# Performance work log

Hardware: AMD Instinct MI355X
Metric: run time of the kernel (lower is better)

Reference implementation:

```python
import jax, jax.numpy as jnp
import numpy as np


def _conv(x, w, b=None, stride=1, pad=0, groups=1):
    out = jax.lax.conv_general_dilated(
        x, w, (stride, stride), [(pad, pad), (pad, pad)],
        feature_group_count=groups,
        dimension_numbers=('NCHW', 'OIHW', 'NCHW'))
    return out if b is None else out + b[None, :, None, None]


def _lrelu(z):
    return jnp.where(z >= 0, z, 0.1 * z)


def _bn(z, g, b, m, v):
    # eval-mode batchnorm, eps=1e-5
    scale = (g / jnp.sqrt(v + 1e-5))[None, :, None, None]
    return (z - m[None, :, None, None]) * scale + b[None, :, None, None]


def setup_inputs() -> dict:
    key = jax.random.key(0)
    ks = jax.random.split(key, 32)
    s = 0.05
    r = lambda k, sh: jax.random.normal(k, sh, jnp.float32) * s
    inp = {}
    inp['x'] = jax.random.normal(ks[0], (4, 64, 256, 256), jnp.float32)
    inp['y'] = jax.random.normal(ks[1], (4, 64, 64, 64), jnp.float32)
    # Encoder convs + BN (eval stats)
    inp['ew1'] = r(ks[2], (128, 64, 3, 3)); inp['eb1'] = r(ks[3], (128,))
    inp['ebn1_g'] = jnp.ones((128,), jnp.float32); inp['ebn1_b'] = jnp.zeros((128,), jnp.float32)
    inp['ebn1_m'] = jnp.zeros((128,), jnp.float32); inp['ebn1_v'] = jnp.ones((128,), jnp.float32)
    inp['ew2'] = r(ks[4], (256, 128, 3, 3)); inp['eb2'] = r(ks[5], (256,))
    inp['ebn2_g'] = jnp.ones((256,), jnp.float32); inp['ebn2_b'] = jnp.zeros((256,), jnp.float32)
    inp['ebn2_m'] = jnp.zeros((256,), jnp.float32); inp['ebn2_v'] = jnp.ones((256,), jnp.float32)
    # Encoder MLP (torch Linear: [out, in])
    inp['mw1'] = r(ks[6], (256, 256)); inp['mb1'] = r(ks[7], (256,))
    inp['mw2'] = r(ks[8], (256, 256)); inp['mb2'] = r(ks[9], (256,))
    # kernel-prediction head (no bias)
    inp['kw1'] = r(ks[10], (128, 256))
    inp['kw2'] = r(ks[11], (64 * 3 * 3, 128))
    # 1x1 conv after dynamic conv
    inp['cw'] = r(ks[12], (64, 64, 1, 1)); inp['cb'] = r(ks[13], (64,))
    # CA layer (reduction=8 -> 256//8 = 32 mid channels, no bias)
    inp['caw1'] = r(ks[14], (32, 64, 1, 1)); inp['caw2'] = r(ks[15], (64, 32, 1, 1))
    # conv1 (3x3) and conv2 (3x3 stride 2)
    inp['c1w'] = r(ks[16], (64, 64, 3, 3)); inp['c1b'] = r(ks[17], (64,))
    inp['c2w'] = r(ks[18], (64, 64, 3, 3)); inp['c2b'] = r(ks[19], (64,))
    # shared ResBlock (two 3x3 convs + residual)
    inp['r1w'] = r(ks[20], (64, 64, 3, 3)); inp['r1b'] = r(ks[21], (64,))
    inp['r2w'] = r(ks[22], (64, 64, 3, 3)); inp['r2b'] = r(ks[23], (64,))
    return inp


def reference(x, y, ew1, eb1, ebn1_g, ebn1_b, ebn1_m, ebn1_v,
              ew2, eb2, ebn2_g, ebn2_b, ebn2_m, ebn2_v,
              mw1, mb1, mw2, mb2, kw1, kw2, cw, cb, caw1, caw2,
              c1w, c1b, c2w, c2b, r1w, r1b, r2w, r2b):
    b, c, h, w = x.shape
    k = 3

    # ---- Encoder(y) -> degradation embedding [b, 256] ----
    f = _lrelu(_bn(_conv(y, ew1, eb1, stride=2, pad=1), ebn1_g, ebn1_b, ebn1_m, ebn1_v))
    f = _lrelu(_bn(_conv(f, ew2, eb2, stride=1, pad=0), ebn2_g, ebn2_b, ebn2_m, ebn2_v))
    f = jnp.mean(f, axis=(2, 3))                       # AdaptiveAvgPool2d(1)
    emb = _lrelu(f @ mw1.T + mb1) @ mw2.T + mb2        # [b, 256]

    # ---- dynamic per-sample depthwise kernel [b*c, 1, k, k] ----
    kern = _lrelu(emb @ kw1.T) @ kw2.T                 # [b, 64*k*k]
    kern = kern.reshape(b * c, 1, k, k)

    # ---- dynamic depthwise conv (groups = b*c) ----
    dyn = _lrelu(_conv(x.reshape(1, b * c, h, w), kern, pad=(k - 1) // 2, groups=b * c))
    dyn = _conv(dyn.reshape(b, c, h, w), cw, cb)       # 1x1 conv

    # ---- channel attention branch ----
    att = jax.nn.relu(_conv(_lrelu(_conv(x, caw1)), caw2))
    da = dyn + x * att

    # ---- DAB body ----
    out = _lrelu(da)
    out = _conv(out, c1w, c1b, pad=1) + x              # [b,64,256,256]

    def resb(z):
        return z + _conv(jax.nn.relu(_conv(z, r1w, r1b, pad=1)), r2w, r2b, pad=1)

    out2 = resb(_conv(out, c2w, c2b, stride=2, pad=1))   # [b,64,128,128]
    out3 = resb(_conv(out2, c2w, c2b, stride=2, pad=1))  # [b,64,64,64]
    return (out, out2, out3)
```

## Files before the change

### kernel.cpp

```cpp
#include <hip/hip_runtime.h>
#include <hip/hip_bf16.h>
#include <cstddef>
#include <cstdint>

#define DEV __device__ __forceinline__

DEV float lrelu_f(float z){ return z >= 0.f ? z : 0.1f*z; }

typedef __bf16 bf16x8 __attribute__((ext_vector_type(8)));
typedef float  f32x4  __attribute__((ext_vector_type(4)));
typedef unsigned short u16x8 __attribute__((ext_vector_type(8)));

DEV unsigned short bf_bits(float v){
    __hip_bfloat16 h = __float2bfloat16(v);
    unsigned short s; __builtin_memcpy(&s, &h, 2); return s;
}
DEV unsigned short bf_bits(__hip_bfloat16 v){
    unsigned short s; __builtin_memcpy(&s, &v, 2); return s;
}
DEV float u16_to_f(unsigned short s){
    unsigned int u = ((unsigned int)s) << 16;
    float f; __builtin_memcpy(&f, &u, 4); return f;
}
DEV int xswz(int bx, int n){ return (bx & 7) * (n >> 3) + (bx >> 3); }

__global__ __launch_bounds__(256) void k_prep_all(
    const float* __restrict__ c1w,
    const float* __restrict__ ew1, const float* __restrict__ bn1g, const float* __restrict__ bn1v,
    const float* __restrict__ ew2, const float* __restrict__ bn2g, const float* __restrict__ bn2v,
    const float* __restrict__ cw, const float* __restrict__ caw1, const float* __restrict__ caw2,
    __hip_bfloat16* __restrict__ wpA, __hip_bfloat16* __restrict__ wp1,
    __hip_bfloat16* __restrict__ wp2, __hip_bfloat16* __restrict__ wpF)
{
    const int blk = blockIdx.x, tid = threadIdx.x;
    if (blk < 144){
        int i = blk*256 + tid;
        int e = i & 7, coA = (i>>3)&63, g = (i>>9)&3, f = i>>11;
        int ch = (f>=9)?1:0, pos = f-9*ch;
        wpA[i] = __float2bfloat16(c1w[coA*576 + (ch*32+g*8+e)*9 + pos]);
    } else if (blk < 432){
        int i = (blk-144)*256 + tid;
        int e = i & 7, co = (i>>3)&127, g = (i>>10)&3, f = i>>12;
        int ch = (f>=9)?1:0, pos = f-9*ch;
        float s = bn1g[co] / sqrtf(bn1v[co] + 1e-5f);
        wp1[i] = __float2bfloat16(ew1[co*576 + (ch*32+g*8+e)*9 + pos] * s);
    } else if (blk < 1584){
        int i = (blk-432)*256 + tid;
        int e = i & 7, co = (i>>3)&255, g = (i>>11)&3, f = i>>13;
        int ch = f/9, pos = f-9*ch;
        float s = bn2g[co] / sqrtf(bn2v[co] + 1e-5f);
        wp2[i] = __float2bfloat16(ew2[co*1152 + (ch*32+g*8+e)*9 + pos] * s);
    } else {
        int i = (blk-1584)*256 + tid;
        if (i < 4096){
            int e = i&7, co = (i>>3)&63, g = (i>>9)&3, ch = i>>11;
            wpF[i] = __float2bfloat16(cw[co*64 + ch*32 + g*8 + e]);
        } else if (i < 6144){
            int j = i - 4096;
            int e = j&7, co = (j>>3)&31, g = (j>>8)&3, ch = j>>10;
            wpF[i] = __float2bfloat16(caw1[co*64 + ch*32 + g*8 + e]);
        } else {
            int j = i - 6144;
            int e = j&7, co = (j>>3)&63, g = j>>9;
            wpF[i] = __float2bfloat16(caw2[co*32 + g*8 + e]);
        }
    }
}

__global__ __launch_bounds__(256) void k_wprepB(
    const float* __restrict__ c2w, const float* __restrict__ r1w,
    const float* __restrict__ r2w, __hip_bfloat16* __restrict__ wpB)
{
    int i = blockIdx.x*256 + threadIdx.x;
    int sel = i / 36864;
    int j   = i - sel*36864;
    const float* w = (sel==0) ? c2w : (sel==1) ? r1w : r2w;
    int e = j & 7, coA = (j>>3)&63, g = (j>>9)&3, f = j>>11;
    int ch = (f>=9)?1:0, pos = f-9*ch;
    wpB[i] = __float2bfloat16(w[coA*576 + (ch*32+g*8+e)*9 + pos]);
}

__global__ __launch_bounds__(256) void k_enc1m(
    const float* __restrict__ y, const __hip_bfloat16* __restrict__ wp1,
    const float* __restrict__ eb1, const float* __restrict__ bng,
    const float* __restrict__ bnb, const float* __restrict__ bnm,
    const float* __restrict__ bnv, __hip_bfloat16* __restrict__ e1b)
{
    __shared__ __align__(16) char lA[9*33*128];
    const int tid = threadIdx.x;
    const int wid = tid >> 6, lane = tid & 63;
    const int l15 = lane & 15, lg = lane >> 4;
    const int b = blockIdx.y, tile = blockIdx.x;
    const int toh = (tile >> 1) * 4;
    const int tow = (tile & 1) * 16;
    const int row0 = toh*2 - 1, col0 = tow*2 - 1;

    for (int i = tid; i < 9*33*64; i += 256){
        int c  = i % 33;
        int t  = i / 33;
        int r  = t % 9;
        int ci = t / 9;
        int ih = row0 + r, iw = col0 + c;
        unsigned short bits = 0;
        if (ih >= 0 && ih < 64 && iw >= 0 && iw < 64)
            bits = bf_bits(y[((size_t)(b*64+ci) << 12) + ih*64 + iw]);
        *(unsigned short*)(lA + ((r*33+c)*8 + ((ci>>3) ^ (c&7)))*16 + (ci&7)*2) = bits;
    }
    __syncthreads();

    f32x4 acc[2][4];
    #pragma unroll
    for (int s = 0; s < 2; ++s)
        #pragma unroll
        for (int n = 0; n < 4; ++n) acc[s][n] = (f32x4){0.f,0.f,0.f,0.f};

    #pragma unroll
    for (int ch = 0; ch < 2; ++ch){
        #pragma unroll
        for (int pos = 0; pos < 9; ++pos){
            const int f = ch*9 + pos;
            const int kh = pos/3, kw = pos - 3*(pos/3);
            bf16x8 bx[4];
            #pragma unroll
            for (int n = 0; n < 4; ++n){
                const int rr = n*2 + kh, cc = l15*2 + kw;
                bx[n] = *(const bf16x8*)(lA + ((rr*33+cc)*8 + ((ch*4+lg) ^ (cc&7)))*16);
            }
            #pragma unroll
            for (int s = 0; s < 2; ++s){
                const int coA = wid*32 + s*16 + l15;
                bf16x8 aw = *(const bf16x8*)(wp1 + ((size_t)(f*4 + lg)*128 + coA)*8);
                #pragma unroll
                for (int n = 0; n < 4; ++n)
                    acc[s][n] = __builtin_amdgcn_mfma_f32_16x16x32_bf16(aw, bx[n], acc[s][n], 0,0,0);
            }
        }
    }

    #pragma unroll
    for (int s = 0; s < 2; ++s){
        #pragma unroll
        for (int r = 0; r < 4; ++r){
            const int co = wid*32 + s*16 + lg*4 + r;
            float sb = bng[co] / sqrtf(bnv[co] + 1e-5f);
            float bs = (eb1[co] - bnm[co])*sb + bnb[co];
            #pragma unroll
            for (int n = 0; n < 4; ++n){
                int oh = toh + n, ow = tow + l15;
                e1b[((size_t)(b*128+co) << 10) + oh*32 + ow]
                    = __float2bfloat16(lrelu_f(acc[s][n][r] + bs));
            }
        }
    }
}

__global__ __launch_bounds__(256) void k_enc2m(
    const __hip_bfloat16* __restrict__ e1b, const __hip_bfloat16* __restrict__ wp2,
    const float* __restrict__ bias, const float* __restrict__ g_,
    const float* __restrict__ bb, const float* __restrict__ m_,
    const float* __restrict__ v_, float* __restrict__ partial)
{
    __shared__ __align__(16) char lA[6*18*16*16];
    const int tid = threadIdx.x;
    const int wid = tid >> 6, lane = tid & 63;
    const int l15 = lane & 15, lg = lane >> 4;
    const int b = blockIdx.y, tile = blockIdx.x;
    const int toh = (tile >> 1) * 4;
    const int tow = (tile & 1) * 16;

    for (int i = tid; i < 13824; i += 256){
        int c  = i % 18;
        int t  = i / 18;
        int r  = t % 6;
        int ci = t / 6;
        int ih = toh + r, iw = tow + c;
        unsigned short bits = 0;
        if (ih < 32 && iw < 32)
            bits = bf_bits(e1b[((size_t)(b*128+ci) << 10) + ih*32 + iw]);
        *(unsigned short*)(lA + ((r*18+c)*16 + ((ci>>3) ^ (c&7)))*16 + (ci&7)*2) = bits;
    }
    __syncthreads();

    f32x4 acc[4][4];
    #pragma unroll
    for (int s = 0; s < 4; ++s)
        #pragma unroll
        for (int n = 0; n < 4; ++n) acc[s][n] = (f32x4){0.f,0.f,0.f,0.f};

    #pragma unroll
    for (int ch = 0; ch < 4; ++ch){
        #pragma unroll
        for (int pos = 0; pos < 9; ++pos){
            const int f = ch*9 + pos;
            const int kh = pos/3, kw = pos - 3*(pos/3);
            bf16x8 bx[4];
            #pragma unroll
            for (int n = 0; n < 4; ++n){
                const int rr = n + kh, cc = l15 + kw;
                bx[n] = *(const bf16x8*)(lA + ((rr*18+cc)*16 + ((ch*4+lg) ^ (cc&7)))*16);
            }
            #pragma unroll
            for (int s = 0; s < 4; ++s){
                const int coA = wid*64 + s*16 + l15;
                bf16x8 aw = *(const bf16x8*)(wp2 + ((size_t)(f*4 + lg)*256 + coA)*8);
                #pragma unroll
                for (int n = 0; n < 4; ++n)
                    acc[s][n] = __builtin_amdgcn_mfma_f32_16x16x32_bf16(aw, bx[n], acc[s][n], 0,0,0);
            }
        }
    }

    const int ow = tow + l15;
    const bool owok = ow < 30;
    #pragma unroll
    for (int s = 0; s < 4; ++s){
        #pragma unroll
        for (int r = 0; r < 4; ++r){
            const int co = wid*64 + s*16 + lg*4 + r;
            float sb = g_[co] / sqrtf(v_[co] + 1e-5f);
            float bs = (bias[co] - m_[co])*sb + bb[co];
            float th = 0.f;
            #pragma unroll
            for (int n = 0; n < 4; ++n){
                if (owok && (toh + n) < 30)
                    th += lrelu_f(acc[s][n][r] + bs);
            }
            th += __shfl_xor(th, 1);
            th += __shfl_xor(th, 2);
            th += __shfl_xor(th, 4);
            th += __shfl_xor(th, 8);
            if (l15 == 0)
                partial[((size_t)(b*16 + tile))*256 + co] = th;
        }
    }
}

__global__ __launch_bounds__(256) void k_mlp(
    const float* __restrict__ partial,
    const float* __restrict__ mw1, const float* __restrict__ mb1,
    const float* __restrict__ mw2, const float* __restrict__ mb2,
    const float* __restrict__ kw1, const float* __restrict__ kw2,
    float* __restrict__ kern)
{
    __shared__ float fs[256], h1[256], emb[256], k1[128];
    int b = blockIdx.x, t = threadIdx.x;
    {
        float s = 0.f;
        #pragma unroll
        for (int tt = 0; tt < 16; ++tt)
            s += partial[((size_t)(b*16 + tt))*256 + t];
        fs[t] = s * (1.f/900.f);
    }
    __syncthreads();
    {
        float acc = mb1[t];
        const float* wr = mw1 + t*256;
        for (int i=0;i<256;++i) acc += fs[i]*wr[i];
        h1[t] = lrelu_f(acc);
    }
    __syncthreads();
    {
        float acc = mb2[t];
        const float* wr = mw2 + t*256;
        for (int i=0;i<256;++i) acc += h1[i]*wr[i];
        emb[t] = acc;
    }
    __syncthreads();
    if (t < 128){
        float acc = 0.f;
        const float* wr = kw1 + t*256;
        for (int i=0;i<256;++i) acc += emb[i]*wr[i];
        k1[t] = lrelu_f(acc);
    }
    __syncthreads();
    for (int o=t; o<576; o+=256){
        float acc = 0.f;
        const float* wr = kw2 + o*128;
        for (int i=0;i<128;++i) acc += k1[i]*wr[i];
        kern[b*576+o] = acc;
    }
}

__global__ __launch_bounds__(256) void k_fuse(
    const float* __restrict__ x, const float* __restrict__ kern,
    const __hip_bfloat16* __restrict__ wpF, const float* __restrict__ cb,
    __hip_bfloat16* __restrict__ buf)
{
    __shared__ __align__(16) char lA [6*18*128];
    __shared__ __align__(16) char lD [64*128];
    __shared__ __align__(16) char lA1[64*64];
    __shared__ float kern_s[576];

    const int tid = threadIdx.x;
    const int wid = tid >> 6, lane = tid & 63;
    const int l15 = lane & 15, lg = lane >> 4;
    const int b = blockIdx.y;
    const int bx = xswz(blockIdx.x, gridDim.x);
    const int toh = (bx >> 4) * 4;
    const int tow = (bx & 15) * 16;
    const int row0 = toh - 1;
    const int col0 = tow - 1;

    const bool cfast = (tow >= 1) && (tow + 20 <= 256);
    for (int i = tid; i < 6*64; i += 256){
        const int ci = i & 63, r = i >> 6;
        const int ih = row0 + r;
        if (ih < 0 || ih >= 256){
            #pragma unroll
            for (int c = 0; c < 18; ++c)
                *(unsigned short*)(lA + ((r*18+c)*8 + ((ci>>3)^(c&7)))*16 + (ci&7)*2) = 0;
        } else {
            const float* srow = x + ((size_t)(b*64+ci) << 16) + ih*256;
            if (cfast){
                float edge = srow[tow-1];
                f32x4 chk[5];
                #pragma unroll
                for (int k = 0; k < 5; ++k)
                    chk[k] = *(const f32x4*)(srow + tow + k*4);
                *(unsigned short*)(lA + ((r*18+0)*8 + ((ci>>3)^0))*16 + (ci&7)*2) = bf_bits(edge);
                #pragma unroll
                for (int c = 1; c < 18; ++c){
                    const int idx = c - 1;
                    unsigned short bits = bf_bits(chk[idx>>2][idx&3]);
                    *(unsigned short*)(lA + ((r*18+c)*8 + ((ci>>3)^(c&7)))*16 + (ci&7)*2) = bits;
                }
            } else {
                #pragma unroll
                for (int c = 0; c < 18; ++c){
                    int iw = col0 + c;
                    unsigned short bits = 0;
                    if (iw >= 0 && iw < 256) bits = bf_bits(srow[iw]);
                    *(unsigned short*)(lA + ((r*18+c)*8 + ((ci>>3)^(c&7)))*16 + (ci&7)*2) = bits;
                }
            }
        }
    }
    for (int i = tid; i < 576; i += 256) kern_s[i] = kern[b*576 + i];
    __syncthreads();

    const int m1 = wid & 1;
    const int nb = (wid >> 1) * 2;
    f32x4 a1acc[2] = {{0.f,0.f,0.f,0.f},{0.f,0.f,0.f,0.f}};
    const int coA1 = m1*16 + l15;
    #pragma unroll
    for (int ch = 0; ch < 2; ++ch){
        bf16x8 aA = *(const bf16x8*)(wpF + 4096 + ((ch*4+lg)*32 + coA1)*8);
        #pragma unroll
        for (int t = 0; t < 2; ++t){
            int n = nb + t;
            int cc = l15 + 1, rr = n + 1;
            bf16x8 bX = *(const bf16x8*)(lA + ((rr*18+cc)*8 + ((ch*4+lg) ^ (cc&7)))*16);
            a1acc[t] = __builtin_amdgcn_mfma_f32_16x16x32_bf16(aA, bX, a1acc[t], 0,0,0);
        }
    }

    {
        const int px = tid & 63;
        const int s0 = tid >> 6;
        const int prow = px >> 4, pcol = px & 15;
        #pragma unroll
        for (int t = 0; t < 2; ++t){
            const int sl = s0 + t*4;
            u16x8 xv[3][3];
            #pragma unroll
            for (int kh = 0; kh < 3; ++kh)
                #pragma unroll
                for (int kw = 0; kw < 3; ++kw){
                    const int r = prow + kh, c = pcol + kw;
                    xv[kh][kw] = *(const u16x8*)(lA + ((r*18+c)*8 + (sl ^ (c&7)))*16);
                }
            u16x8 outv;
            #pragma unroll
            for (int e = 0; e < 8; ++e){
                const int ci = sl*8 + e;
                const float* kr = kern_s + ci*9;
                float acc = 0.f;
                #pragma unroll
                for (int kh = 0; kh < 3; ++kh)
                    #pragma unroll
                    for (int kw = 0; kw < 3; ++kw)
                        acc += u16_to_f(xv[kh][kw][e]) * kr[kh*3+kw];
                outv[e] = bf_bits(lrelu_f(acc));
            }
            *(u16x8*)(lD + (px*8 + (sl ^ (px&7)))*16) = outv;
        }
    }

    #pragma unroll
    for (int t = 0; t < 2; ++t){
        int n = nb + t;
        int px = n*16 + l15;
        #pragma unroll
        for (int r = 0; r < 4; ++r){
            int j = m1*16 + lg*4 + r;
            *(unsigned short*)(lA1 + (px*4 + ((j>>3) ^ (px&3)))*16 + (j&7)*2)
                = bf_bits(lrelu_f(a1acc[t][r]));
        }
    }
    __syncthreads();

    f32x4 dynacc[4] = {{0.f,0.f,0.f,0.f},{0.f,0.f,0.f,0.f},{0.f,0.f,0.f,0.f},{0.f,0.f,0.f,0.f}};
    f32x4 attacc[4] = {{0.f,0.f,0.f,0.f},{0.f,0.f,0.f,0.f},{0.f,0.f,0.f,0.f},{0.f,0.f,0.f,0.f}};
    const int coA = wid*16 + l15;
    #pragma unroll
    for (int ch = 0; ch < 2; ++ch){
        bf16x8 aW = *(const bf16x8*)(wpF + ((ch*4+lg)*64 + coA)*8);
        #pragma unroll
        for (int n = 0; n < 4; ++n){
            int px = n*16 + l15;
            bf16x8 bD = *(const bf16x8*)(lD + (px*8 + ((ch*4+lg) ^ (px&7)))*16);
            dynacc[n] = __builtin_amdgcn_mfma_f32_16x16x32_bf16(aW, bD, dynacc[n], 0,0,0);
        }
    }
    {
        bf16x8 aW2 = *(const bf16x8*)(wpF + 6144 + (lg*64 + coA)*8);
        #pragma unroll
        for (int n = 0; n < 4; ++n){
            int px = n*16 + l15;
            bf16x8 bA1 = *(const bf16x8*)(lA1 + (px*4 + (lg ^ (px&3)))*16);
            attacc[n] = __builtin_amdgcn_mfma_f32_16x16x32_bf16(aW2, bA1, attacc[n], 0,0,0);
        }
    }

    #pragma unroll
    for (int n = 0; n < 4; ++n){
        int oh = toh + n, ow = tow + l15;
        const int rr = n + 1, cc = l15 + 1;
        #pragma unroll
        for (int r = 0; r < 4; ++r){
            int co = wid*16 + lg*4 + r;
            size_t oi = ((size_t)(b*64+co) << 16) + oh*256 + ow;
            float xv = u16_to_f(*(const unsigned short*)(
                lA + ((rr*18+cc)*8 + ((co>>3) ^ (cc&7)))*16 + (co&7)*2));
            float att = fmaxf(attacc[n][r], 0.f);
            float v = lrelu_f(dynacc[n][r] + cb[co] + xv*att);
            buf[oi] = __float2bfloat16(v);
        }
    }
}

template<typename TIN, int STRIDE, int TH, int RESMODE, int ACT, int OUTBF>
__global__ __launch_bounds__(256) void k_conv_mfma(
    const TIN* __restrict__ in, const __hip_bfloat16* __restrict__ wp,
    const float* __restrict__ bias, const void* __restrict__ res,
    void* __restrict__ outp, int H, int W, int Ho, int Wo)
{
    constexpr int ROWS = (STRIDE==1) ? TH+2 : 2*TH+1;
    constexpr int COLS = (STRIDE==1) ? 18 : 33;
    constexpr int EPC  = (sizeof(TIN)==2) ? 8 : 4;
    constexpr int NCH  = (COLS - 1 + EPC - 1) / EPC;
    __shared__ __align__(16) char lA[ROWS*COLS*128];
    const int tid = threadIdx.x;
    const int wid = tid >> 6, lane = tid & 63;
    const int l15 = lane & 15, g = lane >> 4;
    const int b   = blockIdx.y;
    const int bx  = xswz(blockIdx.x, gridDim.x);
    const int tilesW = Wo >> 4;
    const int toh = (bx / tilesW) * TH;
    const int tow = (bx % tilesW) * 16;
    const int row0 = toh*STRIDE - 1;
    const int col0 = tow*STRIDE - 1;

    bf16x8 aw[18];
    const int coA = wid*16 + l15;
    #pragma unroll
    for (int f = 0; f < 18; ++f)
        aw[f] = *(const bf16x8*)(wp + ((f*4 + g)*64 + coA)*8);

    const int base = tow*STRIDE;
    const bool cfast = (base >= 1) && (base + NCH*EPC <= W);
    for (int i = tid; i < ROWS*64; i += 256){
        const int ci = i & 63, r = i >> 6;
        const int ih = row0 + r;
        if (ih < 0 || ih >= H){
            #pragma unroll
            for (int c = 0; c < COLS; ++c)
                *(unsigned short*)(lA + ((r*COLS+c)*8 + ((ci>>3)^(c&7)))*16 + (ci&7)*2) = 0;
        } else {
            const TIN* srow = in + ((size_t)(b*64+ci))*H*W + (size_t)ih*W;
            if (cfast){
                if constexpr (sizeof(TIN) == 2){
                    unsigned short edge = bf_bits(srow[base-1]);
                    u16x8 chk[NCH];
                    #pragma unroll
                    for (int k = 0; k < NCH; ++k)
                        chk[k] = *(const u16x8*)(srow + base + k*8);
                    *(unsigned short*)(lA + ((r*COLS+0)*8 + (ci>>3))*16 + (ci&7)*2) = edge;
                    #pragma unroll
                    for (int c = 1; c < COLS; ++c){
                        const int idx = c - 1;
                        unsigned short bits = chk[idx>>3][idx&7];
                        *(unsigned short*)(lA + ((r*COLS+c)*8 + ((ci>>3)^(c&7)))*16 + (ci&7)*2) = bits;
                    }
                } else {
                    unsigned short edge = bf_bits(srow[base-1]);
                    f32x4 chk[NCH];
                    #pragma unroll
                    for (int k = 0; k < NCH; ++k)
                        chk[k] = *(const f32x4*)(srow + base + k*4);
                    *(unsigned short*)(lA + ((r*COLS+0)*8 + (ci>>3))*16 + (ci&7)*2) = edge;
                    #pragma unroll
                    for (int c = 1; c < COLS; ++c){
                        const int idx = c - 1;
                        unsigned short bits = bf_bits(chk[idx>>2][idx&3]);
                        *(unsigned short*)(lA + ((r*COLS+c)*8 + ((ci>>3)^(c&7)))*16 + (ci&7)*2) = bits;
                    }
                }
            } else {
                #pragma unroll
                for (int c = 0; c < COLS; ++c){
                    int iw = col0 + c;
                    unsigned short bits = 0;
                    if (iw >= 0 && iw < W) bits = bf_bits(srow[iw]);
                    *(unsigned short*)(lA + ((r*COLS+c)*8 + ((ci>>3)^(c&7)))*16 + (ci&7)*2) = bits;
                }
            }
        }
    }
    __syncthreads();

    float bv[4];
    #pragma unroll
    for (int r = 0; r < 4; ++r) bv[r] = bias[wid*16 + g*4 + r];
    const float*          resF = (const float*)res;
    const __hip_bfloat16* resB = (const __hip_bfloat16*)res;

    if constexpr (STRIDE == 1){
        bf16x8 Bw[3][2][3];
        auto ldrow = [&](int rr, int slot){
            #pragma unroll
            for (int ch = 0; ch < 2; ++ch)
                #pragma unroll
                for (int kw = 0; kw < 3; ++kw){
                    const int cc = l15 + kw;
                    Bw[slot][ch][kw] = *(const bf16x8*)(lA + ((rr*COLS + cc)*8 + ((ch*4+g) ^ (cc&7)))*16);
                }
        };
        ldrow(0, 0);
        ldrow(1, 1);
        #pragma unroll
        for (int n = 0; n < TH; ++n){
            ldrow(n+2, (n+2)%3);
            f32x4 acc = {0.f,0.f,0.f,0.f};
            #pragma unroll
            for (int kh = 0; kh < 3; ++kh)
                #pragma unroll
                for (int ch = 0; ch < 2; ++ch)
                    #pragma unroll
                    for (int kw = 0; kw < 3; ++kw)
                        acc = __builtin_amdgcn_mfma_f32_16x16x32_bf16(
                                aw[ch*9 + kh*3 + kw], Bw[(n+kh)%3][ch][kw], acc, 0, 0, 0);
            const int oh = toh + n, ow = tow + l15;
            #pragma unroll
            for (int r = 0; r < 4; ++r){
                int co = wid*16 + g*4 + r;
                size_t oi = ((size_t)(b*64+co)*Ho + oh)*Wo + ow;
                float v = acc[r] + bv[r];
                if (ACT) v = fmaxf(v, 0.f);
                if (RESMODE == 1) v += resF[oi];
                if (RESMODE == 2) v += __bfloat162float(resB[oi]);
                if (OUTBF) ((__hip_bfloat16*)outp)[oi] = __float2bfloat16(v);
                else       ((float*)outp)[oi] = v;
            }
        }
    } else {
        #pragma unroll
        for (int n = 0; n < TH; ++n){
            f32x4 acc = {0.f,0.f,0.f,0.f};
            #pragma unroll
            for (int ch = 0; ch < 2; ++ch)
                #pragma unroll
                for (int pos = 0; pos < 9; ++pos){
                    const int kh = pos/3, kw = pos - 3*(pos/3);
                    const int cc = l15*STRIDE + kw;
                    const int rr = n*STRIDE + kh;
                    bf16x8 bx2 = *(const bf16x8*)(lA + ((rr*COLS + cc)*8 + ((ch*4+g) ^ (cc&7)))*16);
                    acc = __builtin_amdgcn_mfma_f32_16x16x32_bf16(aw[ch*9+pos], bx2, acc, 0, 0, 0);
                }
            const int oh = toh + n, ow = tow + l15;
            #pragma unroll
            for (int r = 0; r < 4; ++r){
                int co = wid*16 + g*4 + r;
                size_t oi = ((size_t)(b*64+co)*Ho + oh)*Wo + ow;
                float v = acc[r] + bv[r];
                if (ACT) v = fmaxf(v, 0.f);
                if (RESMODE == 1) v += resF[oi];
                if (RESMODE == 2) v += __bfloat162float(resB[oi]);
                if (OUTBF) ((__hip_bfloat16*)outp)[oi] = __float2bfloat16(v);
                else       ((float*)outp)[oi] = v;
            }
        }
    }
}

extern "C" void kernel_launch(void* const* d_in, const int* in_sizes, int n_in,
                              void* d_out, int out_size, void* d_ws, size_t ws_size,
                              hipStream_t stream) {
    const float* x    = (const float*)d_in[0];
    const float* y    = (const float*)d_in[1];
    const float* ew1  = (const float*)d_in[2];
    const float* eb1  = (const float*)d_in[3];
    const float* bn1g = (const float*)d_in[4];
    const float* bn1b = (const float*)d_in[5];
    const float* bn1m = (const float*)d_in[6];
    const float* bn1v = (const float*)d_in[7];
    const float* ew2  = (const float*)d_in[8];
    const float* eb2  = (const float*)d_in[9];
    const float* bn2g = (const float*)d_in[10];
    const float* bn2b = (const float*)d_in[11];
    const float* bn2m = (const float*)d_in[12];
    const float* bn2v = (const float*)d_in[13];
    const float* mw1  = (const float*)d_in[14];
    const float* mb1  = (const float*)d_in[15];
    const float* mw2  = (const float*)d_in[16];
    const float* mb2  = (const float*)d_in[17];
    const float* kw1  = (const float*)d_in[18];
    const float* kw2  = (const float*)d_in[19];
    const float* cw   = (const float*)d_in[20];
    const float* cb   = (const float*)d_in[21];
    const float* caw1 = (const float*)d_in[22];
    const float* caw2 = (const float*)d_in[23];
    const float* c1w  = (const float*)d_in[24];
    const float* c1b  = (const float*)d_in[25];
    const float* c2w  = (const float*)d_in[26];
    const float* c2b  = (const float*)d_in[27];
    const float* r1w  = (const float*)d_in[28];
    const float* r1b  = (const float*)d_in[29];
    const float* r2w  = (const float*)d_in[30];
    const float* r2b  = (const float*)d_in[31];

    char* wsc = (char*)d_ws;
    __hip_bfloat16* buf = (__hip_bfloat16*)wsc;
    __hip_bfloat16* e1b = (__hip_bfloat16*)wsc;
    __hip_bfloat16* wp2 = (__hip_bfloat16*)(wsc + 2097152);
    float*          part= (float*)(wsc + 2686976);
    __hip_bfloat16* t2  = (__hip_bfloat16*)wsc;
    __hip_bfloat16* u2  = (__hip_bfloat16*)(wsc + 8388608);
    __hip_bfloat16* t3  = (__hip_bfloat16*)(wsc + 16777216);
    __hip_bfloat16* u3  = (__hip_bfloat16*)(wsc + 18874368);
    __hip_bfloat16* wpB = (__hip_bfloat16*)(wsc + 29360128);
    __hip_bfloat16* wpB0= wpB;
    __hip_bfloat16* wpB1= wpB + 36864;
    __hip_bfloat16* wpB2= wpB + 73728;
    float*          kern= (float*)(wsc + 33558528);

    float* ob   = (float*)d_out;
    float* ob1  = ob + 16777216;
    float* ob2  = ob + 20971520;
    __hip_bfloat16* wpF = (__hip_bfloat16*)((char*)d_out + 83886080);
    __hip_bfloat16* wp1 = (__hip_bfloat16*)((char*)d_out + 84934656);
    __hip_bfloat16* wpA = (__hip_bfloat16*)((char*)d_out + 87932928);

    k_prep_all<<<dim3(1616),256,0,stream>>>(c1w, ew1, bn1g, bn1v, ew2, bn2g, bn2v,
                                            cw, caw1, caw2, wpA, wp1, wp2, wpF);
    k_enc1m<<<dim3(16,4),256,0,stream>>>(y, wp1, eb1, bn1g, bn1b, bn1m, bn1v, e1b);
    k_enc2m<<<dim3(16,4),256,0,stream>>>(e1b, wp2, eb2, bn2g, bn2b, bn2m, bn2v, part);
    k_mlp<<<dim3(4),256,0,stream>>>(part, mw1, mb1, mw2, mb2, kw1, kw2, kern);
    k_fuse<<<dim3(1024,4),256,0,stream>>>(x, kern, wpF, cb, buf);

    k_conv_mfma<__hip_bfloat16,1,8,1,0,0><<<dim3(512,4),256,0,stream>>>(buf, wpA, c1b, x, ob, 256,256,256,256);
    k_wprepB<<<dim3(432),256,0,stream>>>(c2w, r1w, r2w, wpB);
    k_conv_mfma<float,2,2,0,0,1><<<dim3(512,4),256,0,stream>>>(ob, wpB0, c2b, nullptr, t2, 256,256,128,128);
    k_conv_mfma<__hip_bfloat16,1,8,0,1,1><<<dim3(128,4),256,0,stream>>>(t2, wpB1, r1b, nullptr, u2, 128,128,128,128);
    k_conv_mfma<__hip_bfloat16,1,8,2,0,0><<<dim3(128,4),256,0,stream>>>(u2, wpB2, r2b, t2, ob1, 128,128,128,128);
    k_conv_mfma<float,2,2,0,0,1><<<dim3(128,4),256,0,stream>>>(ob1, wpB0, c2b, nullptr, t3, 128,128,64,64);
    k_conv_mfma<__hip_bfloat16,1,8,0,1,1><<<dim3(32,4),256,0,stream>>>(t3, wpB1, r1b, nullptr, u3, 64,64,64,64);
    k_conv_mfma<__hip_bfloat16,1,8,2,0,0><<<dim3(32,4),256,0,stream>>>(u3, wpB2, r2b, t3, ob2, 64,64,64,64);
}
```

Measured before the change: 350.2 us.

## Compute dynamic depthwise conv via block-diagonal MFMA and pad attention LDS rows

Replaces the scalar per-thread depthwise 3x3 convolution in the fused kernel with MFMA instructions. A sparse A operand holds each output channel's kernel tap at a single K position, so each MFMA performs a diagonal (depthwise) product over 16 channels. The attention LDS buffer row stride is also padded from 4 to 5 16-byte slots, presumably to reduce bank conflicts. The MFMA path wastes most of its multiply work on zeros and adds a scattered LDS write pattern for the result, in exchange for removing the per-thread FMA loops and their register pressure.

```diff
diff --git a/kernel.cpp b/kernel.cpp
--- a/kernel.cpp
+++ b/kernel.cpp
@@ -288,7 +288,7 @@
 {
     __shared__ __align__(16) char lA [6*18*128];
     __shared__ __align__(16) char lD [64*128];
-    __shared__ __align__(16) char lA1[64*64];
+    __shared__ __align__(16) char lA1[64*80];
     __shared__ float kern_s[576];
 
     const int tid = threadIdx.x;
@@ -355,34 +355,38 @@
     }
 
     {
-        const int px = tid & 63;
-        const int s0 = tid >> 6;
-        const int prow = px >> 4, pcol = px & 15;
-        #pragma unroll
-        for (int t = 0; t < 2; ++t){
-            const int sl = s0 + t*4;
-            u16x8 xv[3][3];
-            #pragma unroll
-            for (int kh = 0; kh < 3; ++kh)
-                #pragma unroll
-                for (int kw = 0; kw < 3; ++kw){
-                    const int r = prow + kh, c = pcol + kw;
-                    xv[kh][kw] = *(const u16x8*)(lA + ((r*18+c)*8 + (sl ^ (c&7)))*16);
+        const int ch_w = wid >> 1;
+        const int lghit = ((wid & 1) << 1) | (l15 >> 3);
+        const int ehit  = l15 & 7;
+        const int ci_self = wid*16 + l15;
+        const bool lact = (lg == lghit);
+        f32x4 dwc[4] = {{0.f,0.f,0.f,0.f},{0.f,0.f,0.f,0.f},{0.f,0.f,0.f,0.f},{0.f,0.f,0.f,0.f}};
+        #pragma unroll
+        for (int kh = 0; kh < 3; ++kh){
+            #pragma unroll
+            for (int kw = 0; kw < 3; ++kw){
+                unsigned short kv = lact ? bf_bits(kern_s[ci_self*9 + kh*3 + kw]) : (unsigned short)0;
+                u16x8 au;
+                #pragma unroll
+                for (int e = 0; e < 8; ++e) au[e] = (e == ehit) ? kv : (unsigned short)0;
+                bf16x8 adw; __builtin_memcpy(&adw, &au, 16);
+                #pragma unroll
+                for (int n = 0; n < 4; ++n){
+                    const int rr = n + kh, cc = l15 + kw;
+                    bf16x8 bX = *(const bf16x8*)(lA + ((rr*18+cc)*8 + ((ch_w*4+lg) ^ (cc&7)))*16);
+                    dwc[n] = __builtin_amdgcn_mfma_f32_16x16x32_bf16(adw, bX, dwc[n], 0,0,0);
                 }
-            u16x8 outv;
-            #pragma unroll
-            for (int e = 0; e < 8; ++e){
-                const int ci = sl*8 + e;
-                const float* kr = kern_s + ci*9;
-                float acc = 0.f;
-                #pragma unroll
-                for (int kh = 0; kh < 3; ++kh)
-                    #pragma unroll
-                    for (int kw = 0; kw < 3; ++kw)
-                        acc += u16_to_f(xv[kh][kw][e]) * kr[kh*3+kw];
-                outv[e] = bf_bits(lrelu_f(acc));
-            }
-            *(u16x8*)(lD + (px*8 + (sl ^ (px&7)))*16) = outv;
+            }
+        }
+        #pragma unroll
+        for (int n = 0; n < 4; ++n){
+            int px = n*16 + l15;
+            #pragma unroll
+            for (int r = 0; r < 4; ++r){
+                int ci = wid*16 + lg*4 + r;
+                *(unsigned short*)(lD + (px*8 + ((ci>>3) ^ (px&7)))*16 + (ci&7)*2)
+                    = bf_bits(lrelu_f(dwc[n][r]));
+            }
         }
     }
 
@@ -393,7 +397,7 @@
         #pragma unroll
         for (int r = 0; r < 4; ++r){
             int j = m1*16 + lg*4 + r;
-            *(unsigned short*)(lA1 + (px*4 + ((j>>3) ^ (px&3)))*16 + (j&7)*2)
+            *(unsigned short*)(lA1 + (px*5 + ((j>>3) ^ (px&3)))*16 + (j&7)*2)
                 = bf_bits(lrelu_f(a1acc[t][r]));
         }
     }
@@ -417,7 +421,7 @@
         #pragma unroll
         for (int n = 0; n < 4; ++n){
             int px = n*16 + l15;
-            bf16x8 bA1 = *(const bf16x8*)(lA1 + (px*4 + (lg ^ (px&3)))*16);
+            bf16x8 bA1 = *(const bf16x8*)(lA1 + (px*5 + (lg ^ (px&3)))*16);
             attacc[n] = __builtin_amdgcn_mfma_f32_16x16x32_bf16(aW2, bA1, attacc[n], 0,0,0);
         }
     }
```

New measurement: 346.1 us. Within noise of the previous version (-1.2%).
